# Performance work log

Measured on AMD Instinct MI355X. Metric: run time of the kernel, lower is better.

## Reference

```python
import jax, jax.numpy as jnp
import numpy as np

D_MODEL = 1024
NUM_HEADS_Q = 16
NUM_HEADS_KV = 1
D_HEAD = D_MODEL // NUM_HEADS_Q  # 64
KV_DIM = D_HEAD * NUM_HEADS_KV   # 64


def setup_inputs() -> dict:
    key = jax.random.key(0)
    ks = jax.random.split(key, 9)
    b, n = 4, 2048
    s_in = 1.0 / np.sqrt(D_MODEL)
    s_o = 1.0 / np.sqrt(D_MODEL)
    return {
        "x": jax.random.normal(ks[0], (b, n, D_MODEL), jnp.float32),
        # weights stored as [in, out] (= torch Linear weight transposed)
        "W_q": jax.random.uniform(ks[1], (D_MODEL, D_MODEL), jnp.float32, -s_in, s_in),
        "b_q": jax.random.uniform(ks[2], (D_MODEL,), jnp.float32, -s_in, s_in),
        "W_k": jax.random.uniform(ks[3], (D_MODEL, KV_DIM), jnp.float32, -s_in, s_in),
        "b_k": jax.random.uniform(ks[4], (KV_DIM,), jnp.float32, -s_in, s_in),
        "W_v": jax.random.uniform(ks[5], (D_MODEL, KV_DIM), jnp.float32, -s_in, s_in),
        "b_v": jax.random.uniform(ks[6], (KV_DIM,), jnp.float32, -s_in, s_in),
        "W_o": jax.random.uniform(ks[7], (D_MODEL, D_MODEL), jnp.float32, -s_o, s_o),
        "b_o": jax.random.uniform(ks[8], (D_MODEL,), jnp.float32, -s_o, s_o),
    }


def reference(x, W_q, b_q, W_k, b_k, W_v, b_v, W_o, b_o):
    b, n, d_model = x.shape
    # projections
    q = (x @ W_q + b_q).reshape(b, n, NUM_HEADS_Q, D_HEAD).transpose(0, 2, 1, 3)  # [b,hq,n,dh]
    k = (x @ W_k + b_k).reshape(b, n, NUM_HEADS_KV, D_HEAD).transpose(0, 2, 1, 3)  # [b,hkv,n,dh]
    v = (x @ W_v + b_v).reshape(b, n, NUM_HEADS_KV, D_HEAD).transpose(0, 2, 1, 3)
    # MQA: single KV head broadcast over query heads via einsum broadcasting
    scale = 1.0 / np.sqrt(D_HEAD).astype(np.float32)
    # scores [b,hq,n,n]; k/v have hkv=1, broadcast over hq
    scores = jnp.einsum("bhqd,bknd->bhqn", q, k)[..., 0, :, :][:, :, None] if False else None
    # cleaner: squeeze kv head (num_heads_kv == 1)
    k1 = k[:, 0]  # [b,n,dh]
    v1 = v[:, 0]  # [b,n,dh]
    scores = jnp.einsum("bhqd,bkd->bhqk", q, k1) * scale  # [b,hq,n,n]
    attn = jax.nn.softmax(scores, axis=-1)
    out = jnp.einsum("bhqk,bkd->bhqd", attn, v1)  # [b,hq,n,dh]
    out = out.transpose(0, 2, 1, 3).reshape(b, n, d_model)
    return out @ W_o + b_o
```

## Files before the change

### kernel.cpp

```cpp
#include <hip/hip_runtime.h>

using bf16x8 = __attribute__((ext_vector_type(8))) short;
using f32x4  = __attribute__((ext_vector_type(4))) float;
using f32x16 = __attribute__((ext_vector_type(16))) float;
using u32x2  = __attribute__((ext_vector_type(2))) unsigned int;
using u32x4  = __attribute__((ext_vector_type(4))) unsigned int;

__device__ __forceinline__ unsigned short f2bf(float f) {
  unsigned int u = __float_as_uint(f);
  u = u + 0x7fffu + ((u >> 16) & 1u);
  return (unsigned short)(u >> 16);
}

#if __has_builtin(__builtin_amdgcn_exp2f)
#define EXP2(x) __builtin_amdgcn_exp2f(x)
#else
#define EXP2(x) __expf((x) * 0.69314718056f)
#endif

__device__ __forceinline__ unsigned int cvt_pk_bf16(float lo, float hi) {
  unsigned int r;
  asm("v_cvt_pk_bf16_f32 %0, %1, %2" : "=v"(r) : "v"(lo), "v"(hi));
  return r;
}

#define GLL16(SRC, DST) __builtin_amdgcn_global_load_lds( \
    (const __attribute__((address_space(1))) unsigned int*)(SRC), \
    (__attribute__((address_space(3))) unsigned int*)(DST), 16, 0, 0)

__global__ __launch_bounds__(256) void cvt_all_kernel(
    const float* __restrict__ x, unsigned short* __restrict__ xb,
    const float* __restrict__ Wq, const float* __restrict__ Wk,
    const float* __restrict__ Wv, const float* __restrict__ Wo,
    unsigned short* __restrict__ wqkvt, unsigned short* __restrict__ wot) {
  __shared__ float tile[32][33];
  const int bx = blockIdx.x;
  if (bx < 8192) {
    const int i = bx * 256 + threadIdx.x;
    const float4 v = reinterpret_cast<const float4*>(x)[i];
    ushort2 o0 = { f2bf(v.x), f2bf(v.y) };
    ushort2 o1 = { f2bf(v.z), f2bf(v.w) };
    reinterpret_cast<ushort2*>(xb)[2 * i]     = o0;
    reinterpret_cast<ushort2*>(xb)[2 * i + 1] = o1;
    return;
  }
  const float* W; unsigned short* Wt; int N, bi;
  if (bx < 9216)      { W = Wq; Wt = wqkvt;                        N = 1024; bi = bx - 8192; }
  else if (bx < 9280) { W = Wk; Wt = wqkvt + (size_t)1024 * 1024;  N = 64;   bi = bx - 9216; }
  else if (bx < 9344) { W = Wv; Wt = wqkvt + (size_t)1088 * 1024;  N = 64;   bi = bx - 9280; }
  else                { W = Wo; Wt = wot;                          N = 1024; bi = bx - 9344; }
  const int nb = N >> 5;
  const int n0 = (bi % nb) * 32, k0 = (bi / nb) * 32;
  const int tx = threadIdx.x & 31, ty = threadIdx.x >> 5;
  #pragma unroll
  for (int i = 0; i < 32; i += 8)
    tile[ty + i][tx] = W[(size_t)(k0 + ty + i) * N + n0 + tx];
  __syncthreads();
  #pragma unroll
  for (int i = 0; i < 32; i += 8)
    Wt[(size_t)(n0 + ty + i) * 1024 + k0 + tx] = f2bf(tile[tx][ty + i]);
}

template<int MODE>
__global__ __launch_bounds__(256) void gemm_kernel(
    const unsigned short* __restrict__ A, const unsigned short* __restrict__ Bt,
    const float* __restrict__ bias0, const float* __restrict__ bias1,
    const float* __restrict__ bias2,
    void* __restrict__ out0, void* __restrict__ out1, void* __restrict__ out2,
    int K, int N) {
  __shared__ __align__(16) unsigned short alds[2][128 * 32];
  __shared__ __align__(16) unsigned short blds[2][128 * 32];

  const int t    = threadIdx.x;
  const int lane = t & 63;
  const int wid  = t >> 6;
  const int lr = lane & 15, lg = lane >> 4;
  const int row0 = blockIdx.x * 128;
  const int col0 = blockIdx.y * 128;

  const size_t ldb = (size_t)K * 2;
  const char* Ag = (const char*)A  + (size_t)(row0 + (t >> 2)) * ldb + ((t & 3) << 4);
  const char* Bg = (const char*)Bt + (size_t)(col0 + (t >> 2)) * ldb + ((t & 3) << 4);
  char* adst = (char*)alds[0] + wid * 1024;
  char* bdst = (char*)blds[0] + wid * 1024;

  auto stage = [&](int buf, int k0) {
    const size_t kb = (size_t)k0 * 2;
    #pragma unroll
    for (int c = 0; c < 2; ++c) {
      GLL16(Ag + (size_t)c * 64 * ldb + kb, adst + buf * 8192 + c * 4096);
      GLL16(Bg + (size_t)c * 64 * ldb + kb, bdst + buf * 8192 + c * 4096);
    }
  };

  f32x4 acc[4][4];
  #pragma unroll
  for (int i = 0; i < 4; ++i)
    #pragma unroll
    for (int j = 0; j < 4; ++j)
      #pragma unroll
      for (int r = 0; r < 4; ++r) acc[i][j][r] = 0.f;

  stage(0, 0);
  __syncthreads();

  for (int step = 0; step < 32; ++step) {
    const int cur = step & 1;
    if (step < 31) stage(cur ^ 1, (step + 1) * 32);

    const char* ab = (const char*)alds[cur] + (wid >> 1) * 4096;
    const char* bb = (const char*)blds[cur] + (wid & 1) * 4096;
    bf16x8 am[4], bn[4];
    #pragma unroll
    for (int i = 0; i < 4; ++i)
      am[i] = *reinterpret_cast<const bf16x8*>(ab + (i * 16 + lr) * 64 + lg * 16);
    #pragma unroll
    for (int j = 0; j < 4; ++j)
      bn[j] = *reinterpret_cast<const bf16x8*>(bb + (j * 16 + lr) * 64 + lg * 16);
    #pragma unroll
    for (int i = 0; i < 4; ++i)
      #pragma unroll
      for (int j = 0; j < 4; ++j)
        acc[i][j] = __builtin_amdgcn_mfma_f32_16x16x32_bf16(am[i], bn[j], acc[i][j], 0, 0, 0);

    __syncthreads();
  }

  const int wrow0 = row0 + (wid >> 1) * 64;
  const int wcol0 = col0 + (wid & 1) * 64;
  #pragma unroll
  for (int i = 0; i < 4; ++i) {
    #pragma unroll
    for (int j = 0; j < 4; ++j) {
      const int col = wcol0 + j * 16 + lr;
      float bias;
      if constexpr (MODE == 0)
        bias = (col < 1024) ? bias0[col] : ((col < 1088) ? bias1[col - 1024] : bias2[col - 1088]);
      else
        bias = bias0[col];
      #pragma unroll
      for (int r = 0; r < 4; ++r) {
        const int row = wrow0 + i * 16 + lg * 4 + r;
        float v = acc[i][j][r] + bias;
        if constexpr (MODE == 0) {
          const int b = row >> 11, n = row & 2047;
          if (col < 1024) {
            v *= 0.180336880111f;
            const int h = col >> 6, d = col & 63;
            ((unsigned short*)out0)[(((b * 16 + h) * 2048) + n) * 64 + d] = f2bf(v);
          } else if (col < 1088) {
            ((unsigned short*)out1)[row * 64 + (col - 1024)] = f2bf(v);
          } else {
            const int np = (n & ~15) | (n & 3) | ((n & 4) << 1) | ((n & 8) >> 1);
            ((unsigned short*)out2)[(b * 64 + (col - 1088)) * 2048 + np] = f2bf(v);
          }
        } else {
          ((float*)out0)[(size_t)row * N + col] = v;
        }
      }
    }
  }
}

__global__ __launch_bounds__(512, 4) void attn_kernel(
    const unsigned short* __restrict__ Q,
    const unsigned short* __restrict__ Kb,
    const unsigned short* __restrict__ Vt,
    unsigned short* __restrict__ Ao) {
  __shared__ __align__(16) unsigned short klds[2][64 * 64];
  __shared__ __align__(16) unsigned short vlds[2][64 * 64];

  const int lane = threadIdx.x & 63;
  const int wid  = threadIdx.x >> 6;
  const int la = lane & 31, hi = lane >> 5;
  const int swz = (la & 7) << 4;
  const int bh = blockIdx.y, b = bh >> 4, h = bh & 15;
  const int q0 = blockIdx.x * 256 + wid * 32;

  const unsigned short* Qb = Q + (size_t)bh * 2048 * 64;
  const char* Kbase = (const char*)(Kb + (size_t)b * 2048 * 64);
  const char* Vbase = (const char*)(Vt + (size_t)b * 64 * 2048);

  const int srow  = lane >> 3;
  const int schnk = (lane & 7) ^ srow;
  const int krow  = wid * 8 + srow;
  const int koff_lane = krow * 128  + schnk * 16;
  const int voff_lane = krow * 4096 + schnk * 16;
  char* kdst = (char*)klds[0] + wid * 1024;
  char* vdst = (char*)vlds[0] + wid * 1024;

  auto stage = [&](int buf, int kt) {
    GLL16(Kbase + (size_t)kt * 8192 + koff_lane, kdst + buf * 8192);
    GLL16(Vbase + (size_t)kt * 128  + voff_lane, vdst + buf * 8192);
  };

  bf16x8 qa[4];
  #pragma unroll
  for (int kc = 0; kc < 4; ++kc)
    qa[kc] = *reinterpret_cast<const bf16x8*>(&Qb[(q0 + la) * 64 + kc * 16 + hi * 8]);

  float lsum = 0.f;
  f32x16 o[2];
  #pragma unroll
  for (int dt = 0; dt < 2; ++dt)
    #pragma unroll
    for (int r = 0; r < 16; ++r) o[dt][r] = 0.f;

  stage(0, 0);
  __syncthreads();

  for (int kt = 0; kt < 32; ++kt) {
    const int cur = kt & 1;
    if (kt < 31) stage(cur ^ 1, kt + 1);

    const char* kb8 = (const char*)klds[cur];
    const char* vb8 = (const char*)vlds[cur];

    #pragma unroll
    for (int ct = 0; ct < 2; ++ct) {
      f32x16 s;
      #pragma unroll
      for (int r = 0; r < 16; ++r) s[r] = 0.f;
      __builtin_amdgcn_s_setprio(1);
      #pragma unroll
      for (int kc = 0; kc < 4; ++kc) {
        const bf16x8 kf = *reinterpret_cast<const bf16x8*>(
            kb8 + ((ct * 32 + la) << 7) + ((((kc << 1) + hi) << 4) ^ swz));
        s = __builtin_amdgcn_mfma_f32_32x32x16_bf16(kf, qa[kc], s, 0, 0, 0);
      }
      __builtin_amdgcn_s_setprio(0);

      unsigned int W[4][2];
      float ps = 0.f;
      #pragma unroll
      for (int r2 = 0; r2 < 4; ++r2) {
        const float p0 = EXP2(s[r2 * 4 + 0]);
        const float p1 = EXP2(s[r2 * 4 + 1]);
        const float p2 = EXP2(s[r2 * 4 + 2]);
        const float p3 = EXP2(s[r2 * 4 + 3]);
        ps += (p0 + p1) + (p2 + p3);
        W[r2][0] = cvt_pk_bf16(p0, p1);
        W[r2][1] = cvt_pk_bf16(p2, p3);
      }
      lsum += ps;

      __builtin_amdgcn_s_setprio(1);
      #pragma unroll
      for (int ks = 0; ks < 2; ++ks) {
        u32x4 pwv;
        pwv[0] = W[2 * ks][0];
        pwv[1] = W[2 * ks][1];
        pwv[2] = W[2 * ks + 1][0];
        pwv[3] = W[2 * ks + 1][1];
        const bf16x8 pb = __builtin_bit_cast(bf16x8, pwv);
        #pragma unroll
        for (int dt = 0; dt < 2; ++dt) {
          const bf16x8 vf = *reinterpret_cast<const bf16x8*>(
              vb8 + ((dt * 32 + la) << 7) + (((((ct * 2 + ks) << 1) + hi) << 4) ^ swz));
          o[dt] = __builtin_amdgcn_mfma_f32_32x32x16_bf16(vf, pb, o[dt], 0, 0, 0);
        }
      }
      __builtin_amdgcn_s_setprio(0);
    }

    __syncthreads();
  }

  lsum += __shfl_xor(lsum, 32);
  const float inv = 1.f / lsum;
  const size_t rowoff = (size_t)(b * 2048 + q0 + la) * 1024 + h * 64 + hi * 4;
  #pragma unroll
  for (int dt = 0; dt < 2; ++dt) {
    #pragma unroll
    for (int r2 = 0; r2 < 4; ++r2) {
      u32x2 w;
      w[0] = cvt_pk_bf16(o[dt][r2 * 4 + 0] * inv, o[dt][r2 * 4 + 1] * inv);
      w[1] = cvt_pk_bf16(o[dt][r2 * 4 + 2] * inv, o[dt][r2 * 4 + 3] * inv);
      *(u32x2*)(Ao + rowoff + dt * 32 + r2 * 8) = w;
    }
  }
}

extern "C" void kernel_launch(void* const* d_in, const int* in_sizes, int n_in,
                              void* d_out, int out_size, void* d_ws, size_t ws_size,
                              hipStream_t stream) {
  const float* x  = (const float*)d_in[0];
  const float* Wq = (const float*)d_in[1];
  const float* bq = (const float*)d_in[2];
  const float* Wk = (const float*)d_in[3];
  const float* bk = (const float*)d_in[4];
  const float* Wv = (const float*)d_in[5];
  const float* bv = (const float*)d_in[6];
  const float* Wo = (const float*)d_in[7];
  const float* bo = (const float*)d_in[8];
  float* out = (float*)d_out;

  char* ws = (char*)d_ws;
  size_t off = 0;
  auto alloc = [&](size_t bytes) -> void* {
    void* p = ws + off;
    off += (bytes + 255) & ~(size_t)255;
    return p;
  };
  unsigned short* xb    = (unsigned short*)alloc((size_t)8192 * 1024 * 2);
  unsigned short* wqkvt = (unsigned short*)alloc((size_t)1152 * 1024 * 2);
  unsigned short* wot   = (unsigned short*)alloc((size_t)1024 * 1024 * 2);
  unsigned short* qb    = (unsigned short*)alloc((size_t)8192 * 1024 * 2);
  unsigned short* kb    = (unsigned short*)alloc((size_t)8192 * 64 * 2);
  unsigned short* vt    = (unsigned short*)alloc((size_t)4 * 64 * 2048 * 2);
  unsigned short* ao    = (unsigned short*)alloc((size_t)8192 * 1024 * 2);

  cvt_all_kernel<<<10368, 256, 0, stream>>>(x, xb, Wq, Wk, Wv, Wo, wqkvt, wot);
  gemm_kernel<0><<<dim3(64, 9), 256, 0, stream>>>(xb, wqkvt, bq, bk, bv, qb, kb, vt, 1024, 1152);
  attn_kernel<<<dim3(8, 64), 512, 0, stream>>>(qb, kb, vt, ao);
  gemm_kernel<2><<<dim3(64, 8), 256, 0, stream>>>(ao, wot, bo, nullptr, nullptr, out, nullptr, nullptr, 1024, 1024);
}
```

Before: 153.8 us.

## Process two query tiles per wave in attention to reuse K/V LDS fragments

Each attention wave now handles 64 query rows as two 32-row groups instead of 32 rows, so every K and V fragment read from LDS feeds two MFMAs. The block shrinks from 8 to 4 waves, and each wave stages twice as many K/V rows per tile. The k-loop is also unrolled by two with fixed buffer indices. The aim is to cut LDS read traffic and loop overhead per MFMA. In exchange there is more register pressure (double accumulators and Q fragments) and fewer waves per CU to hide latency.

```diff
diff --git a/kernel.cpp b/kernel.cpp
--- a/kernel.cpp
+++ b/kernel.cpp
@@ -162,7 +162,7 @@
   }
 }
 
-__global__ __launch_bounds__(512, 4) void attn_kernel(
+__global__ __launch_bounds__(256, 2) void attn_kernel(
     const unsigned short* __restrict__ Q,
     const unsigned short* __restrict__ Kb,
     const unsigned short* __restrict__ Vt,
@@ -175,7 +175,7 @@
   const int la = lane & 31, hi = lane >> 5;
   const int swz = (la & 7) << 4;
   const int bh = blockIdx.y, b = bh >> 4, h = bh & 15;
-  const int q0 = blockIdx.x * 256 + wid * 32;
+  const int q0 = blockIdx.x * 256 + wid * 64;
 
   const unsigned short* Qb = Q + (size_t)bh * 2048 * 64;
   const char* Kbase = (const char*)(Kb + (size_t)b * 2048 * 64);
@@ -183,100 +183,121 @@
 
   const int srow  = lane >> 3;
   const int schnk = (lane & 7) ^ srow;
-  const int krow  = wid * 8 + srow;
-  const int koff_lane = krow * 128  + schnk * 16;
-  const int voff_lane = krow * 4096 + schnk * 16;
-  char* kdst = (char*)klds[0] + wid * 1024;
-  char* vdst = (char*)vlds[0] + wid * 1024;
+  const int koff0 = (wid * 16 + 0 + srow) * 128  + schnk * 16;
+  const int koff1 = (wid * 16 + 8 + srow) * 128  + schnk * 16;
+  const int voff0 = (wid * 16 + 0 + srow) * 4096 + schnk * 16;
+  const int voff1 = (wid * 16 + 8 + srow) * 4096 + schnk * 16;
+  char* kdst = (char*)klds[0] + wid * 2048;
+  char* vdst = (char*)vlds[0] + wid * 2048;
 
   auto stage = [&](int buf, int kt) {
-    GLL16(Kbase + (size_t)kt * 8192 + koff_lane, kdst + buf * 8192);
-    GLL16(Vbase + (size_t)kt * 128  + voff_lane, vdst + buf * 8192);
+    GLL16(Kbase + (size_t)kt * 8192 + koff0, kdst + buf * 8192);
+    GLL16(Kbase + (size_t)kt * 8192 + koff1, kdst + buf * 8192 + 1024);
+    GLL16(Vbase + (size_t)kt * 128  + voff0, vdst + buf * 8192);
+    GLL16(Vbase + (size_t)kt * 128  + voff1, vdst + buf * 8192 + 1024);
   };
 
-  bf16x8 qa[4];
-  #pragma unroll
-  for (int kc = 0; kc < 4; ++kc)
-    qa[kc] = *reinterpret_cast<const bf16x8*>(&Qb[(q0 + la) * 64 + kc * 16 + hi * 8]);
-
-  float lsum = 0.f;
-  f32x16 o[2];
-  #pragma unroll
-  for (int dt = 0; dt < 2; ++dt)
-    #pragma unroll
-    for (int r = 0; r < 16; ++r) o[dt][r] = 0.f;
-
-  stage(0, 0);
-  __syncthreads();
-
-  for (int kt = 0; kt < 32; ++kt) {
-    const int cur = kt & 1;
-    if (kt < 31) stage(cur ^ 1, kt + 1);
-
-    const char* kb8 = (const char*)klds[cur];
-    const char* vb8 = (const char*)vlds[cur];
-
+  bf16x8 qa[2][4];
+  #pragma unroll
+  for (int qg = 0; qg < 2; ++qg)
+    #pragma unroll
+    for (int kc = 0; kc < 4; ++kc)
+      qa[qg][kc] = *reinterpret_cast<const bf16x8*>(
+          &Qb[(q0 + qg * 32 + la) * 64 + kc * 16 + hi * 8]);
+
+  float lsum[2] = {0.f, 0.f};
+  f32x16 o[2][2];
+  #pragma unroll
+  for (int qg = 0; qg < 2; ++qg)
+    #pragma unroll
+    for (int dt = 0; dt < 2; ++dt)
+      #pragma unroll
+      for (int r = 0; r < 16; ++r) o[qg][dt][r] = 0.f;
+
+  auto body = [&](const char* kb8, const char* vb8) {
     #pragma unroll
     for (int ct = 0; ct < 2; ++ct) {
-      f32x16 s;
-      #pragma unroll
-      for (int r = 0; r < 16; ++r) s[r] = 0.f;
+      f32x16 s0, s1;
+      #pragma unroll
+      for (int r = 0; r < 16; ++r) { s0[r] = 0.f; s1[r] = 0.f; }
       __builtin_amdgcn_s_setprio(1);
       #pragma unroll
       for (int kc = 0; kc < 4; ++kc) {
         const bf16x8 kf = *reinterpret_cast<const bf16x8*>(
             kb8 + ((ct * 32 + la) << 7) + ((((kc << 1) + hi) << 4) ^ swz));
-        s = __builtin_amdgcn_mfma_f32_32x32x16_bf16(kf, qa[kc], s, 0, 0, 0);
+        s0 = __builtin_amdgcn_mfma_f32_32x32x16_bf16(kf, qa[0][kc], s0, 0, 0, 0);
+        s1 = __builtin_amdgcn_mfma_f32_32x32x16_bf16(kf, qa[1][kc], s1, 0, 0, 0);
       }
       __builtin_amdgcn_s_setprio(0);
 
-      unsigned int W[4][2];
-      float ps = 0.f;
+      unsigned int W0[4][2], W1[4][2];
+      float ps0 = 0.f, ps1 = 0.f;
       #pragma unroll
       for (int r2 = 0; r2 < 4; ++r2) {
-        const float p0 = EXP2(s[r2 * 4 + 0]);
-        const float p1 = EXP2(s[r2 * 4 + 1]);
-        const float p2 = EXP2(s[r2 * 4 + 2]);
-        const float p3 = EXP2(s[r2 * 4 + 3]);
-        ps += (p0 + p1) + (p2 + p3);
-        W[r2][0] = cvt_pk_bf16(p0, p1);
-        W[r2][1] = cvt_pk_bf16(p2, p3);
-      }
-      lsum += ps;
+        const float a0 = EXP2(s0[r2 * 4 + 0]), a1 = EXP2(s0[r2 * 4 + 1]);
+        const float a2 = EXP2(s0[r2 * 4 + 2]), a3 = EXP2(s0[r2 * 4 + 3]);
+        ps0 += (a0 + a1) + (a2 + a3);
+        W0[r2][0] = cvt_pk_bf16(a0, a1);
+        W0[r2][1] = cvt_pk_bf16(a2, a3);
+        const float c0 = EXP2(s1[r2 * 4 + 0]), c1 = EXP2(s1[r2 * 4 + 1]);
+        const float c2 = EXP2(s1[r2 * 4 + 2]), c3 = EXP2(s1[r2 * 4 + 3]);
+        ps1 += (c0 + c1) + (c2 + c3);
+        W1[r2][0] = cvt_pk_bf16(c0, c1);
+        W1[r2][1] = cvt_pk_bf16(c2, c3);
+      }
+      lsum[0] += ps0;
+      lsum[1] += ps1;
 
       __builtin_amdgcn_s_setprio(1);
       #pragma unroll
       for (int ks = 0; ks < 2; ++ks) {
-        u32x4 pwv;
-        pwv[0] = W[2 * ks][0];
-        pwv[1] = W[2 * ks][1];
-        pwv[2] = W[2 * ks + 1][0];
-        pwv[3] = W[2 * ks + 1][1];
-        const bf16x8 pb = __builtin_bit_cast(bf16x8, pwv);
+        u32x4 w0, w1;
+        w0[0] = W0[2 * ks][0]; w0[1] = W0[2 * ks][1];
+        w0[2] = W0[2 * ks + 1][0]; w0[3] = W0[2 * ks + 1][1];
+        w1[0] = W1[2 * ks][0]; w1[1] = W1[2 * ks][1];
+        w1[2] = W1[2 * ks + 1][0]; w1[3] = W1[2 * ks + 1][1];
+        const bf16x8 pb0 = __builtin_bit_cast(bf16x8, w0);
+        const bf16x8 pb1 = __builtin_bit_cast(bf16x8, w1);
         #pragma unroll
         for (int dt = 0; dt < 2; ++dt) {
           const bf16x8 vf = *reinterpret_cast<const bf16x8*>(
               vb8 + ((dt * 32 + la) << 7) + (((((ct * 2 + ks) << 1) + hi) << 4) ^ swz));
-          o[dt] = __builtin_amdgcn_mfma_f32_32x32x16_bf16(vf, pb, o[dt], 0, 0, 0);
+          o[0][dt] = __builtin_amdgcn_mfma_f32_32x32x16_bf16(vf, pb0, o[0][dt], 0, 0, 0);
+          o[1][dt] = __builtin_amdgcn_mfma_f32_32x32x16_bf16(vf, pb1, o[1][dt], 0, 0, 0);
         }
       }
       __builtin_amdgcn_s_setprio(0);
     }
-
+  };
+
+  stage(0, 0);
+  __syncthreads();
+
+  #pragma unroll 1
+  for (int t2 = 0; t2 < 16; ++t2) {
+    stage(1, 2 * t2 + 1);
+    body((const char*)klds[0], (const char*)vlds[0]);
     __syncthreads();
-  }
-
-  lsum += __shfl_xor(lsum, 32);
-  const float inv = 1.f / lsum;
-  const size_t rowoff = (size_t)(b * 2048 + q0 + la) * 1024 + h * 64 + hi * 4;
-  #pragma unroll
-  for (int dt = 0; dt < 2; ++dt) {
-    #pragma unroll
-    for (int r2 = 0; r2 < 4; ++r2) {
-      u32x2 w;
-      w[0] = cvt_pk_bf16(o[dt][r2 * 4 + 0] * inv, o[dt][r2 * 4 + 1] * inv);
-      w[1] = cvt_pk_bf16(o[dt][r2 * 4 + 2] * inv, o[dt][r2 * 4 + 3] * inv);
-      *(u32x2*)(Ao + rowoff + dt * 32 + r2 * 8) = w;
+    if (t2 < 15) stage(0, 2 * t2 + 2);
+    body((const char*)klds[1], (const char*)vlds[1]);
+    __syncthreads();
+  }
+
+  #pragma unroll
+  for (int qg = 0; qg < 2; ++qg) {
+    float l = lsum[qg];
+    l += __shfl_xor(l, 32);
+    const float inv = 1.f / l;
+    const size_t rowoff = (size_t)(b * 2048 + q0 + qg * 32 + la) * 1024 + h * 64 + hi * 4;
+    #pragma unroll
+    for (int dt = 0; dt < 2; ++dt) {
+      #pragma unroll
+      for (int r2 = 0; r2 < 4; ++r2) {
+        u32x2 w;
+        w[0] = cvt_pk_bf16(o[qg][dt][r2 * 4 + 0] * inv, o[qg][dt][r2 * 4 + 1] * inv);
+        w[1] = cvt_pk_bf16(o[qg][dt][r2 * 4 + 2] * inv, o[qg][dt][r2 * 4 + 3] * inv);
+        *(u32x2*)(Ao + rowoff + dt * 32 + r2 * 8) = w;
+      }
     }
   }
 }
@@ -312,6 +333,6 @@
 
   cvt_all_kernel<<<10368, 256, 0, stream>>>(x, xb, Wq, Wk, Wv, Wo, wqkvt, wot);
   gemm_kernel<0><<<dim3(64, 9), 256, 0, stream>>>(xb, wqkvt, bq, bk, bv, qb, kb, vt, 1024, 1152);
-  attn_kernel<<<dim3(8, 64), 512, 0, stream>>>(qb, kb, vt, ao);
+  attn_kernel<<<dim3(8, 64), 256, 0, stream>>>(qb, kb, vt, ao);
   gemm_kernel<2><<<dim3(64, 8), 256, 0, stream>>>(ao, wot, bo, nullptr, nullptr, out, nullptr, nullptr, 1024, 1024);
 }
```

New measurement: 150.6 us. 1.02x faster.
